# Kernel tuning notes

Hardware: AMD Instinct MI355X
Metric: run time of the kernel (lower is better)

The kernel has to match this reference:

```python
import jax, jax.numpy as jnp
import numpy as np

N = 10000          # num nodes
E = 640000         # num edges (avg degree 64)
IN_CH = 128
OUT_CH = 128


def setup_inputs() -> dict:
    key = jax.random.key(0)
    k_x, k_ei, k_ea, k_w1, k_b1, k_w2, k_b2 = jax.random.split(key, 7)
    x = jax.random.normal(k_x, (N, IN_CH), dtype=jnp.float32)
    edge_index = jax.random.randint(k_ei, (2, E), 0, N, dtype=jnp.int64)
    edge_attr = jax.random.uniform(k_ea, (E,), dtype=jnp.float32)
    # MLP params: Linear(2*in, out) -> ReLU -> Linear(out, out), stored as [in, out]
    s1 = 1.0 / np.sqrt(2 * IN_CH)
    s2 = 1.0 / np.sqrt(OUT_CH)
    W1 = jax.random.uniform(k_w1, (2 * IN_CH, OUT_CH), jnp.float32, -s1, s1)
    b1 = jax.random.uniform(k_b1, (OUT_CH,), jnp.float32, -s1, s1)
    W2 = jax.random.uniform(k_w2, (OUT_CH, OUT_CH), jnp.float32, -s2, s2)
    b2 = jax.random.uniform(k_b2, (OUT_CH,), jnp.float32, -s2, s2)
    return {"x": x, "edge_index": edge_index, "edge_attr": edge_attr,
            "W1": W1, "b1": b1, "W2": W2, "b2": b2}


def reference(x, edge_index, edge_attr, W1, b1, W2, b2):
    row, col = edge_index[0], edge_index[1]
    # message: scale sender feature by edge_attr, concat with receiver feature, 2-layer MLP
    x_i = x[row] * edge_attr[:, None]          # [E, in]
    x_j = x[col]                               # [E, in]
    combined = jnp.concatenate([x_i, x_j], axis=1)  # [E, 2*in]
    h = jax.nn.relu(combined @ W1 + b1)        # [E, out]
    messages = h @ W2 + b2                     # [E, out]
    # sum aggregation: scatter-add messages into receiving nodes (col)
    out = jnp.zeros((x.shape[0], messages.shape[1]), dtype=messages.dtype)
    out = out.at[col].add(messages)
    return out
```

## Files before the change

kernel.cpp:

```cpp
#include <hip/hip_runtime.h>

#define C 128
#define NPB 16
#define CAP 128
#define OVF_MAX 65536
#define CSTRIDE 16
#define EPT 8

__device__ __forceinline__ unsigned bf16_bits(float x) {
    unsigned u = __float_as_uint(x);
    u += 0x7FFFu + ((u >> 16) & 1u);
    return u >> 16;
}
__device__ __forceinline__ float bf16f(unsigned short b) {
    return __uint_as_float(((unsigned)b) << 16);
}

__global__ void fused_pre_kernel(const float* __restrict__ x, const float* __restrict__ W1,
                                 unsigned short* __restrict__ P16, float* __restrict__ Q,
                                 const int* __restrict__ ei, const float* __restrict__ attr,
                                 int* __restrict__ cursor, int* __restrict__ ovf_cnt,
                                 int2* __restrict__ ovf, unsigned* __restrict__ sorted,
                                 int N, int E, int SB) {
    if ((int)blockIdx.x < SB) {
        const int base = (blockIdx.x * 256 + threadIdx.x) * EPT;
        if (base >= E) return;
        if (base + EPT <= E) {
            const int4 r0 = *(const int4*)(ei + base);
            const int4 r1 = *(const int4*)(ei + base + 4);
            const int4 c0 = *(const int4*)(ei + (size_t)E + base);
            const int4 c1 = *(const int4*)(ei + (size_t)E + base + 4);
            const float4 a0 = *(const float4*)(attr + base);
            const float4 a1 = *(const float4*)(attr + base + 4);
            const int rows[EPT] = {r0.x, r0.y, r0.z, r0.w, r1.x, r1.y, r1.z, r1.w};
            const int cols[EPT] = {c0.x, c0.y, c0.z, c0.w, c1.x, c1.y, c1.z, c1.w};
            const float as[EPT] = {a0.x, a0.y, a0.z, a0.w, a1.x, a1.y, a1.z, a1.w};
            int pos[EPT];
#pragma unroll
            for (int j = 0; j < EPT; ++j)
                pos[j] = atomicAdd(&cursor[cols[j] * CSTRIDE], 1);
#pragma unroll
            for (int j = 0; j < EPT; ++j) {
                const unsigned v = (bf16_bits(as[j]) << 16) | (unsigned)rows[j];
                if (pos[j] < CAP) {
                    sorted[(size_t)cols[j] * CAP + pos[j]] = v;
                } else {
                    const int o = atomicAdd(ovf_cnt, 1);
                    if (o < OVF_MAX) ovf[o] = make_int2(cols[j], (int)v);
                }
            }
        } else {
            for (int e = base; e < E; ++e) {
                const int row = ei[e], colv = ei[(size_t)E + e];
                const int pos = atomicAdd(&cursor[colv * CSTRIDE], 1);
                const unsigned v = (bf16_bits(attr[e]) << 16) | (unsigned)row;
                if (pos < CAP) sorted[(size_t)colv * CAP + pos] = v;
                else {
                    const int o = atomicAdd(ovf_cnt, 1);
                    if (o < OVF_MAX) ovf[o] = make_int2(colv, (int)v);
                }
            }
        }
    } else {
        __shared__ float xs[NPB][C];
        const int pb = blockIdx.x - SB;
        const int n0 = pb * NPB;
        const int tt = threadIdx.x & (C - 1);
        const int half = threadIdx.x >> 7;
        for (int i = threadIdx.x; i < NPB * C; i += 256) {
            const int gi = n0 * C + i;
            xs[0][i] = (gi < N * C) ? x[gi] : 0.f;
        }
        __syncthreads();
        const float* __restrict__ Wb = W1 + (half ? (C * C) : 0) + tt;
        float acc[NPB] = {};
        for (int k = 0; k < C; ++k) {
            const float w = Wb[k * C];
#pragma unroll
            for (int j = 0; j < NPB; ++j)
                acc[j] = fmaf(xs[j][k], w, acc[j]);
        }
#pragma unroll
        for (int j = 0; j < NPB; ++j)
            if (n0 + j < N) {
                if (half) Q[(size_t)(n0 + j) * C + tt] = acc[j];
                else      P16[(size_t)(n0 + j) * C + tt] = (unsigned short)bf16_bits(acc[j]);
            }
    }
}

__global__ void agg_out_kernel(const unsigned* __restrict__ sorted, const int* __restrict__ cursor,
                               const unsigned short* __restrict__ P16, const float* __restrict__ Q,
                               const float* __restrict__ b1, const float* __restrict__ W2,
                               const float* __restrict__ b2,
                               const int* __restrict__ ovf_cnt, const int2* __restrict__ ovf,
                               float* __restrict__ out, int N) {
    __shared__ float4 part[2][4][32];
    __shared__ float hs[2][C];
    const int t = threadIdx.x;
    const int j = t >> 7;
    const int slice = (t >> 5) & 3;
    const int ch4 = t & 31;
    const int n = blockIdx.x * 2 + j;

    float4 acc = make_float4(0.f, 0.f, 0.f, 0.f);
    float4 qb = acc;
    int deg = 0;
    if (n < N) {
        deg = cursor[n * CSTRIDE];
        const float4 q4  = *(const float4*)(Q + (size_t)n * C + (ch4 << 2));
        const float4 b14 = *(const float4*)(b1 + (ch4 << 2));
        qb = make_float4(q4.x + b14.x, q4.y + b14.y, q4.z + b14.z, q4.w + b14.w);
        const int cnt = min(deg, CAP);
        const unsigned* __restrict__ buf = sorted + (size_t)n * CAP;
        const int chunk = (cnt + 3) >> 2;
        const int s0 = min(slice * chunk, cnt);
        const int s1 = min(s0 + chunk, cnt);
        int i = s0;
        for (; i + 4 <= s1; i += 4) {
            const unsigned v0 = buf[i], v1 = buf[i + 1], v2 = buf[i + 2], v3 = buf[i + 3];
            const ushort4 p0 = *(const ushort4*)(P16 + (((size_t)(v0 & 0xFFFFu)) << 7) + (ch4 << 2));
            const ushort4 p1 = *(const ushort4*)(P16 + (((size_t)(v1 & 0xFFFFu)) << 7) + (ch4 << 2));
            const ushort4 p2 = *(const ushort4*)(P16 + (((size_t)(v2 & 0xFFFFu)) << 7) + (ch4 << 2));
            const ushort4 p3 = *(const ushort4*)(P16 + (((size_t)(v3 & 0xFFFFu)) << 7) + (ch4 << 2));
            const float a0 = __uint_as_float(v0 & 0xFFFF0000u);
            const float a1 = __uint_as_float(v1 & 0xFFFF0000u);
            const float a2 = __uint_as_float(v2 & 0xFFFF0000u);
            const float a3 = __uint_as_float(v3 & 0xFFFF0000u);
            acc.x += fmaxf(fmaf(a0, bf16f(p0.x), qb.x), 0.f) + fmaxf(fmaf(a1, bf16f(p1.x), qb.x), 0.f)
                   + fmaxf(fmaf(a2, bf16f(p2.x), qb.x), 0.f) + fmaxf(fmaf(a3, bf16f(p3.x), qb.x), 0.f);
            acc.y += fmaxf(fmaf(a0, bf16f(p0.y), qb.y), 0.f) + fmaxf(fmaf(a1, bf16f(p1.y), qb.y), 0.f)
                   + fmaxf(fmaf(a2, bf16f(p2.y), qb.y), 0.f) + fmaxf(fmaf(a3, bf16f(p3.y), qb.y), 0.f);
            acc.z += fmaxf(fmaf(a0, bf16f(p0.z), qb.z), 0.f) + fmaxf(fmaf(a1, bf16f(p1.z), qb.z), 0.f)
                   + fmaxf(fmaf(a2, bf16f(p2.z), qb.z), 0.f) + fmaxf(fmaf(a3, bf16f(p3.z), qb.z), 0.f);
            acc.w += fmaxf(fmaf(a0, bf16f(p0.w), qb.w), 0.f) + fmaxf(fmaf(a1, bf16f(p1.w), qb.w), 0.f)
                   + fmaxf(fmaf(a2, bf16f(p2.w), qb.w), 0.f) + fmaxf(fmaf(a3, bf16f(p3.w), qb.w), 0.f);
        }
        for (; i < s1; ++i) {
            const unsigned v = buf[i];
            const ushort4 p = *(const ushort4*)(P16 + (((size_t)(v & 0xFFFFu)) << 7) + (ch4 << 2));
            const float a = __uint_as_float(v & 0xFFFF0000u);
            acc.x += fmaxf(fmaf(a, bf16f(p.x), qb.x), 0.f);
            acc.y += fmaxf(fmaf(a, bf16f(p.y), qb.y), 0.f);
            acc.z += fmaxf(fmaf(a, bf16f(p.z), qb.z), 0.f);
            acc.w += fmaxf(fmaf(a, bf16f(p.w), qb.w), 0.f);
        }
        if (slice == 0) {
            const int oc = min(*ovf_cnt, OVF_MAX);
            for (int o = 0; o < oc; ++o) {
                const int2 v = ovf[o];
                if (v.x == n) {
                    const unsigned u = (unsigned)v.y;
                    const ushort4 p = *(const ushort4*)(P16 + (((size_t)(u & 0xFFFFu)) << 7) + (ch4 << 2));
                    const float a = __uint_as_float(u & 0xFFFF0000u);
                    acc.x += fmaxf(fmaf(a, bf16f(p.x), qb.x), 0.f);
                    acc.y += fmaxf(fmaf(a, bf16f(p.y), qb.y), 0.f);
                    acc.z += fmaxf(fmaf(a, bf16f(p.z), qb.z), 0.f);
                    acc.w += fmaxf(fmaf(a, bf16f(p.w), qb.w), 0.f);
                }
            }
        }
    }
    part[j][slice][ch4] = acc;
    __syncthreads();
    if (slice == 0 && n < N) {
        const float4 r0 = part[j][0][ch4], r1 = part[j][1][ch4];
        const float4 r2 = part[j][2][ch4], r3 = part[j][3][ch4];
        float4 h;
        h.x = r0.x + r1.x + r2.x + r3.x;
        h.y = r0.y + r1.y + r2.y + r3.y;
        h.z = r0.z + r1.z + r2.z + r3.z;
        h.w = r0.w + r1.w + r2.w + r3.w;
        *(float4*)(&hs[j][ch4 << 2]) = h;
    }
    __syncthreads();
    float4 o = make_float4(0.f, 0.f, 0.f, 0.f);
    if (n < N) {
        const int k0 = slice << 5;
#pragma unroll 8
        for (int k = k0; k < k0 + 32; ++k) {
            const float hv = hs[j][k];
            const float4 w = *(const float4*)(W2 + (size_t)k * C + (ch4 << 2));
            o.x = fmaf(hv, w.x, o.x);
            o.y = fmaf(hv, w.y, o.y);
            o.z = fmaf(hv, w.z, o.z);
            o.w = fmaf(hv, w.w, o.w);
        }
    }
    __syncthreads();
    part[j][slice][ch4] = o;
    __syncthreads();
    if (slice == 0 && n < N) {
        const float4 r0 = part[j][0][ch4], r1 = part[j][1][ch4];
        const float4 r2 = part[j][2][ch4], r3 = part[j][3][ch4];
        const float4 b24 = *(const float4*)(b2 + (ch4 << 2));
        const float d = (float)deg;
        float4 res;
        res.x = fmaf(d, b24.x, r0.x + r1.x + r2.x + r3.x);
        res.y = fmaf(d, b24.y, r0.y + r1.y + r2.y + r3.y);
        res.z = fmaf(d, b24.z, r0.z + r1.z + r2.z + r3.z);
        res.w = fmaf(d, b24.w, r0.w + r1.w + r2.w + r3.w);
        *(float4*)(out + (size_t)n * C + (ch4 << 2)) = res;
    }
}

extern "C" void kernel_launch(void* const* d_in, const int* in_sizes, int n_in,
                              void* d_out, int out_size, void* d_ws, size_t ws_size,
                              hipStream_t stream) {
    const float* x    = (const float*)d_in[0];
    const int*   ei   = (const int*)d_in[1];
    const float* attr = (const float*)d_in[2];
    const float* W1   = (const float*)d_in[3];
    const float* b1   = (const float*)d_in[4];
    const float* W2   = (const float*)d_in[5];
    const float* b2   = (const float*)d_in[6];
    float* out = (float*)d_out;

    const int N = in_sizes[0] / C;
    const int E = in_sizes[2];

    char* ws = (char*)d_ws;
    unsigned short* P16 = (unsigned short*)ws;  ws += (size_t)N * C * sizeof(unsigned short);
    ws = (char*)(((uintptr_t)ws + 15) & ~(uintptr_t)15);
    float*    Q       = (float*)ws;     ws += (size_t)N * C * sizeof(float);
    unsigned* sorted  = (unsigned*)ws;  ws += (size_t)N * CAP * sizeof(unsigned);
    int2*     ovf     = (int2*)ws;      ws += (size_t)OVF_MAX * sizeof(int2);
    int*      cursor  = (int*)ws;       ws += (size_t)N * CSTRIDE * sizeof(int);
    int*      ovf_cnt = (int*)ws;

    hipMemsetAsync(cursor, 0, ((size_t)N * CSTRIDE + 1) * sizeof(int), stream);

    const int SB = (E + 256 * EPT - 1) / (256 * EPT);
    const int PB = (N + NPB - 1) / NPB;
    fused_pre_kernel<<<SB + PB, 256, 0, stream>>>(x, W1, P16, Q, ei, attr,
                                                  cursor, ovf_cnt, ovf, sorted, N, E, SB);
    agg_out_kernel<<<(N + 1) / 2, 256, 0, stream>>>(sorted, cursor, P16, Q, b1, W2, b2,
                                                    ovf_cnt, ovf, out, N);
}
```

Baseline: 158.2 us.

## Split per-node edge buckets into eight slabs by block to cut atomic contention

The edge bucketing now spreads each destination node's edges over eight slabs, picked by block index. Each slab has its own cursor array, laid out contiguously instead of padded to 16-int stride, and its own 24-entry bucket. The aggregation kernel sums the eight counts and each of the four slices walks two slabs with vectorized uint4 index loads. The aim is to spread atomic contention and shrink the cursor array, at the cost of possible overflow when a slab holds more than 24 edges (about 8 expected per slab at degree 64). It also makes per-slice work less balanced than the old even split of one bucket.

Result: no change. 159.2 us (+0.6%).

```diff
diff --git a/kernel.cpp b/kernel.cpp
--- a/kernel.cpp
+++ b/kernel.cpp
@@ -2,9 +2,9 @@
 
 #define C 128
 #define NPB 16
-#define CAP 128
+#define NSLAB 8
+#define CAP8 24
 #define OVF_MAX 65536
-#define CSTRIDE 16
 #define EPT 8
 
 __device__ __forceinline__ unsigned bf16_bits(float x) {
@@ -23,6 +23,9 @@
                                  int2* __restrict__ ovf, unsigned* __restrict__ sorted,
                                  int N, int E, int SB) {
     if ((int)blockIdx.x < SB) {
+        const int slab = blockIdx.x & (NSLAB - 1);
+        int* __restrict__ cur = cursor + (size_t)slab * N;
+        unsigned* __restrict__ sl = sorted + (size_t)slab * N * CAP8;
         const int base = (blockIdx.x * 256 + threadIdx.x) * EPT;
         if (base >= E) return;
         if (base + EPT <= E) {
@@ -38,12 +41,12 @@
             int pos[EPT];
 #pragma unroll
             for (int j = 0; j < EPT; ++j)
-                pos[j] = atomicAdd(&cursor[cols[j] * CSTRIDE], 1);
+                pos[j] = atomicAdd(&cur[cols[j]], 1);
 #pragma unroll
             for (int j = 0; j < EPT; ++j) {
                 const unsigned v = (bf16_bits(as[j]) << 16) | (unsigned)rows[j];
-                if (pos[j] < CAP) {
-                    sorted[(size_t)cols[j] * CAP + pos[j]] = v;
+                if (pos[j] < CAP8) {
+                    sl[(size_t)cols[j] * CAP8 + pos[j]] = v;
                 } else {
                     const int o = atomicAdd(ovf_cnt, 1);
                     if (o < OVF_MAX) ovf[o] = make_int2(cols[j], (int)v);
@@ -52,9 +55,9 @@
         } else {
             for (int e = base; e < E; ++e) {
                 const int row = ei[e], colv = ei[(size_t)E + e];
-                const int pos = atomicAdd(&cursor[colv * CSTRIDE], 1);
+                const int pos = atomicAdd(&cur[colv], 1);
                 const unsigned v = (bf16_bits(attr[e]) << 16) | (unsigned)row;
-                if (pos < CAP) sorted[(size_t)colv * CAP + pos] = v;
+                if (pos < CAP8) sl[(size_t)colv * CAP8 + pos] = v;
                 else {
                     const int o = atomicAdd(ovf_cnt, 1);
                     if (o < OVF_MAX) ovf[o] = make_int2(colv, (int)v);
@@ -107,43 +110,49 @@
     float4 qb = acc;
     int deg = 0;
     if (n < N) {
-        deg = cursor[n * CSTRIDE];
+        int cnts[NSLAB];
+#pragma unroll
+        for (int s = 0; s < NSLAB; ++s) {
+            cnts[s] = cursor[(size_t)s * N + n];
+            deg += cnts[s];
+        }
         const float4 q4  = *(const float4*)(Q + (size_t)n * C + (ch4 << 2));
         const float4 b14 = *(const float4*)(b1 + (ch4 << 2));
         qb = make_float4(q4.x + b14.x, q4.y + b14.y, q4.z + b14.z, q4.w + b14.w);
-        const int cnt = min(deg, CAP);
-        const unsigned* __restrict__ buf = sorted + (size_t)n * CAP;
-        const int chunk = (cnt + 3) >> 2;
-        const int s0 = min(slice * chunk, cnt);
-        const int s1 = min(s0 + chunk, cnt);
-        int i = s0;
-        for (; i + 4 <= s1; i += 4) {
-            const unsigned v0 = buf[i], v1 = buf[i + 1], v2 = buf[i + 2], v3 = buf[i + 3];
-            const ushort4 p0 = *(const ushort4*)(P16 + (((size_t)(v0 & 0xFFFFu)) << 7) + (ch4 << 2));
-            const ushort4 p1 = *(const ushort4*)(P16 + (((size_t)(v1 & 0xFFFFu)) << 7) + (ch4 << 2));
-            const ushort4 p2 = *(const ushort4*)(P16 + (((size_t)(v2 & 0xFFFFu)) << 7) + (ch4 << 2));
-            const ushort4 p3 = *(const ushort4*)(P16 + (((size_t)(v3 & 0xFFFFu)) << 7) + (ch4 << 2));
-            const float a0 = __uint_as_float(v0 & 0xFFFF0000u);
-            const float a1 = __uint_as_float(v1 & 0xFFFF0000u);
-            const float a2 = __uint_as_float(v2 & 0xFFFF0000u);
-            const float a3 = __uint_as_float(v3 & 0xFFFF0000u);
-            acc.x += fmaxf(fmaf(a0, bf16f(p0.x), qb.x), 0.f) + fmaxf(fmaf(a1, bf16f(p1.x), qb.x), 0.f)
-                   + fmaxf(fmaf(a2, bf16f(p2.x), qb.x), 0.f) + fmaxf(fmaf(a3, bf16f(p3.x), qb.x), 0.f);
-            acc.y += fmaxf(fmaf(a0, bf16f(p0.y), qb.y), 0.f) + fmaxf(fmaf(a1, bf16f(p1.y), qb.y), 0.f)
-                   + fmaxf(fmaf(a2, bf16f(p2.y), qb.y), 0.f) + fmaxf(fmaf(a3, bf16f(p3.y), qb.y), 0.f);
-            acc.z += fmaxf(fmaf(a0, bf16f(p0.z), qb.z), 0.f) + fmaxf(fmaf(a1, bf16f(p1.z), qb.z), 0.f)
-                   + fmaxf(fmaf(a2, bf16f(p2.z), qb.z), 0.f) + fmaxf(fmaf(a3, bf16f(p3.z), qb.z), 0.f);
-            acc.w += fmaxf(fmaf(a0, bf16f(p0.w), qb.w), 0.f) + fmaxf(fmaf(a1, bf16f(p1.w), qb.w), 0.f)
-                   + fmaxf(fmaf(a2, bf16f(p2.w), qb.w), 0.f) + fmaxf(fmaf(a3, bf16f(p3.w), qb.w), 0.f);
-        }
-        for (; i < s1; ++i) {
-            const unsigned v = buf[i];
-            const ushort4 p = *(const ushort4*)(P16 + (((size_t)(v & 0xFFFFu)) << 7) + (ch4 << 2));
-            const float a = __uint_as_float(v & 0xFFFF0000u);
-            acc.x += fmaxf(fmaf(a, bf16f(p.x), qb.x), 0.f);
-            acc.y += fmaxf(fmaf(a, bf16f(p.y), qb.y), 0.f);
-            acc.z += fmaxf(fmaf(a, bf16f(p.z), qb.z), 0.f);
-            acc.w += fmaxf(fmaf(a, bf16f(p.w), qb.w), 0.f);
+#pragma unroll
+        for (int si = 0; si < 2; ++si) {
+            const int s = slice + (si << 2);
+            const int cs = min(cnts[s], CAP8);
+            const unsigned* __restrict__ buf = sorted + ((size_t)s * N + n) * CAP8;
+            int i = 0;
+            for (; i + 4 <= cs; i += 4) {
+                const uint4 v = *(const uint4*)(buf + i);
+                const ushort4 p0 = *(const ushort4*)(P16 + (((size_t)(v.x & 0xFFFFu)) << 7) + (ch4 << 2));
+                const ushort4 p1 = *(const ushort4*)(P16 + (((size_t)(v.y & 0xFFFFu)) << 7) + (ch4 << 2));
+                const ushort4 p2 = *(const ushort4*)(P16 + (((size_t)(v.z & 0xFFFFu)) << 7) + (ch4 << 2));
+                const ushort4 p3 = *(const ushort4*)(P16 + (((size_t)(v.w & 0xFFFFu)) << 7) + (ch4 << 2));
+                const float a0 = __uint_as_float(v.x & 0xFFFF0000u);
+                const float a1 = __uint_as_float(v.y & 0xFFFF0000u);
+                const float a2 = __uint_as_float(v.z & 0xFFFF0000u);
+                const float a3 = __uint_as_float(v.w & 0xFFFF0000u);
+                acc.x += fmaxf(fmaf(a0, bf16f(p0.x), qb.x), 0.f) + fmaxf(fmaf(a1, bf16f(p1.x), qb.x), 0.f)
+                       + fmaxf(fmaf(a2, bf16f(p2.x), qb.x), 0.f) + fmaxf(fmaf(a3, bf16f(p3.x), qb.x), 0.f);
+                acc.y += fmaxf(fmaf(a0, bf16f(p0.y), qb.y), 0.f) + fmaxf(fmaf(a1, bf16f(p1.y), qb.y), 0.f)
+                       + fmaxf(fmaf(a2, bf16f(p2.y), qb.y), 0.f) + fmaxf(fmaf(a3, bf16f(p3.y), qb.y), 0.f);
+                acc.z += fmaxf(fmaf(a0, bf16f(p0.z), qb.z), 0.f) + fmaxf(fmaf(a1, bf16f(p1.z), qb.z), 0.f)
+                       + fmaxf(fmaf(a2, bf16f(p2.z), qb.z), 0.f) + fmaxf(fmaf(a3, bf16f(p3.z), qb.z), 0.f);
+                acc.w += fmaxf(fmaf(a0, bf16f(p0.w), qb.w), 0.f) + fmaxf(fmaf(a1, bf16f(p1.w), qb.w), 0.f)
+                       + fmaxf(fmaf(a2, bf16f(p2.w), qb.w), 0.f) + fmaxf(fmaf(a3, bf16f(p3.w), qb.w), 0.f);
+            }
+            for (; i < cs; ++i) {
+                const unsigned v = buf[i];
+                const ushort4 p = *(const ushort4*)(P16 + (((size_t)(v & 0xFFFFu)) << 7) + (ch4 << 2));
+                const float a = __uint_as_float(v & 0xFFFF0000u);
+                acc.x += fmaxf(fmaf(a, bf16f(p.x), qb.x), 0.f);
+                acc.y += fmaxf(fmaf(a, bf16f(p.y), qb.y), 0.f);
+                acc.z += fmaxf(fmaf(a, bf16f(p.z), qb.z), 0.f);
+                acc.w += fmaxf(fmaf(a, bf16f(p.w), qb.w), 0.f);
+            }
         }
         if (slice == 0) {
             const int oc = min(*ovf_cnt, OVF_MAX);
@@ -223,12 +232,12 @@
     unsigned short* P16 = (unsigned short*)ws;  ws += (size_t)N * C * sizeof(unsigned short);
     ws = (char*)(((uintptr_t)ws + 15) & ~(uintptr_t)15);
     float*    Q       = (float*)ws;     ws += (size_t)N * C * sizeof(float);
-    unsigned* sorted  = (unsigned*)ws;  ws += (size_t)N * CAP * sizeof(unsigned);
+    unsigned* sorted  = (unsigned*)ws;  ws += (size_t)NSLAB * N * CAP8 * sizeof(unsigned);
     int2*     ovf     = (int2*)ws;      ws += (size_t)OVF_MAX * sizeof(int2);
-    int*      cursor  = (int*)ws;       ws += (size_t)N * CSTRIDE * sizeof(int);
+    int*      cursor  = (int*)ws;       ws += (size_t)NSLAB * N * sizeof(int);
     int*      ovf_cnt = (int*)ws;
 
-    hipMemsetAsync(cursor, 0, ((size_t)N * CSTRIDE + 1) * sizeof(int), stream);
+    hipMemsetAsync(cursor, 0, ((size_t)NSLAB * N + 1) * sizeof(int), stream);
 
     const int SB = (E + 256 * EPT - 1) / (256 * EPT);
     const int PB = (N + NPB - 1) / NPB;
```
